# Optimization experiments

Hardware: AMD Instinct MI355X
Metric: run time of the kernel (lower is better)

## Reference

```python
import jax, jax.numpy as jnp
import numpy as np

N_NODES = 100000


def _gcn_conv(h, src, dst, W, b, n_nodes):
    """PyG GCNConv with add_self_loops=True, symmetric normalization.
    out = D^-1/2 (A + I) D^-1/2 (h W) + b, aggregating src->dst."""
    h = h @ W  # transform first (out_dim <= in_dim), as PyG does
    ones = jnp.ones(src.shape[0], dtype=h.dtype)
    deg = jax.ops.segment_sum(ones, dst, num_segments=n_nodes) + 1.0  # +1 self loop
    dinv = jax.lax.rsqrt(deg)
    coef = dinv[src] * dinv[dst]  # per-edge norm
    agg = jax.ops.segment_sum(h[src] * coef[:, None], dst, num_segments=n_nodes)
    agg = agg + h * (dinv * dinv)[:, None]  # self-loop term: dinv_i^2 * h_i
    return agg + b


def setup_inputs() -> dict:
    key = jax.random.key(0)
    k1, k2, k3, k4 = jax.random.split(key, 4)
    x = jax.random.normal(k1, (N_NODES, 256), dtype=jnp.float32)
    edge_index = jax.random.randint(k2, (2, 1600000), 0, N_NODES, dtype=jnp.int64)
    W1 = jax.random.normal(k3, (256, 128), dtype=jnp.float32) * (1.0 / np.sqrt(256))
    b1 = jnp.zeros((128,), dtype=jnp.float32)
    W2 = jax.random.normal(k4, (128, 64), dtype=jnp.float32) * (1.0 / np.sqrt(128))
    b2 = jnp.zeros((64,), dtype=jnp.float32)
    return {"x": x, "edge_index": edge_index, "W1": W1, "b1": b1, "W2": W2, "b2": b2}


def reference(x, edge_index, W1, b1, W2, b2):
    src, dst = edge_index[0], edge_index[1]
    h = jax.nn.relu(_gcn_conv(x, src, dst, W1, b1, N_NODES))
    # dropout is identity in eval mode
    h = _gcn_conv(h, src, dst, W2, b2, N_NODES)
    return jax.nn.log_softmax(h, axis=1)
```

## Files before the change

### kernel.cpp

```cpp
#include <hip/hip_runtime.h>
#include <hip/hip_bf16.h>


#define N_NODES 100000
#define F_IN 256
#define F_MID 128
#define F_OUT 64

#define BSHIFT 8
#define BNODES 256
#define NBUCKETS ((N_NODES + BNODES - 1) / BNODES)
#define BCAP 6144
#define EPB 4096

typedef __attribute__((ext_vector_type(8))) short short8;
typedef __attribute__((ext_vector_type(4))) float f32x4;

__device__ inline ushort bf16_rne(float f) {
    uint u = __float_as_uint(f);
    u += 0x7FFF + ((u >> 16) & 1);
    return (ushort)(u >> 16);
}
__device__ inline float lo16(uint r) { return __uint_as_float(r << 16); }
__device__ inline float hi16(uint r) { return __uint_as_float(r & 0xffff0000u); }
__device__ inline uint pack_bf2(float a, float b) {
    return (uint)bf16_rne(a) | ((uint)bf16_rne(b) << 16);
}

__global__ __launch_bounds__(256)
void bucket_sort_kernel(const uint* __restrict__ ebuf, const int* __restrict__ bcur,
                        int* __restrict__ ssrc, int* __restrict__ rs, int* __restrict__ cnt,
                        float* __restrict__ dinv, int n) {
    __shared__ uint eL[BCAP];
    __shared__ int  sLoc[BCAP];
    __shared__ int hist[BNODES], ps[BNODES];
    int b = blockIdx.x, t = threadIdx.x;
    int nb = bcur[b];
    if (nb > BCAP) nb = BCAP;
    for (int i = t; i < nb; i += 256) eL[i] = ebuf[(size_t)b * BCAP + i];
    hist[t] = 0;
    __syncthreads();
    for (int i = t; i < nb; i += 256) atomicAdd(&hist[eL[i] >> 17], 1);
    __syncthreads();
    ps[t] = hist[t];
    __syncthreads();
#pragma unroll
    for (int off = 1; off < BNODES; off <<= 1) {
        int v = (t >= off) ? ps[t - off] : 0;
        __syncthreads();
        ps[t] += v;
        __syncthreads();
    }
    int excl = ps[t] - hist[t];
    int node = b * BNODES + t;
    if (node < n) {
        rs[node] = b * BCAP + excl;
        cnt[node] = hist[t];
        dinv[node] = 1.0f / sqrtf((float)hist[t] + 1.0f);
    }
    __syncthreads();
    ps[t] = excl;
    __syncthreads();
    for (int i = t; i < nb; i += 256) {
        uint e = eL[i];
        int d = e >> 17;
        int p = atomicAdd(&ps[d], 1);
        sLoc[p] = (int)(e & 0x1FFFF);
    }
    __syncthreads();
    for (int i = t; i < nb; i += 256) ssrc[(size_t)b * BCAP + i] = sLoc[i];
}

__global__ __launch_bounds__(256)
void wprep_kernel(const float* __restrict__ W1, const float* __restrict__ W2,
                  short8* __restrict__ W1f, short8* __restrict__ W2f) {
    int b = blockIdx.x;
    if (b < 16) {
        int f = b * 256 + threadIdx.x;
        int k0 = f >> 9, nt = (f >> 6) & 7, ln = f & 63;
        int kbase = k0 * 32 + (ln >> 4) * 8;
        int n = nt * 16 + (ln & 15);
        short8 fr;
#pragma unroll
        for (int j = 0; j < 8; ++j) fr[j] = (short)bf16_rne(W1[(kbase + j) * F_MID + n]);
        W1f[f] = fr;
    } else {
        int f = (b - 16) * 256 + threadIdx.x;
        int k0 = f >> 8, nt = (f >> 6) & 3, ln = f & 63;
        int kbase = k0 * 32 + (ln >> 4) * 8;
        int n = nt * 16 + (ln & 15);
        short8 fr;
#pragma unroll
        for (int j = 0; j < 8; ++j) fr[j] = (short)bf16_rne(W2[(kbase + j) * F_OUT + n]);
        W2f[f] = fr;
    }
}

__global__ __launch_bounds__(512, 4)
void sg_kernel(const int* __restrict__ src, const int* __restrict__ dst,
               int* __restrict__ bcur, uint* __restrict__ ebuf, int E,
               const float* __restrict__ A, const short8* __restrict__ Wf,
               ushort* __restrict__ C, int M, int nScat) {
    __shared__ __align__(16) char smemRaw[32768];
    int t = threadIdx.x;

    if ((int)blockIdx.x < nScat) {
        int* hist = (int*)smemRaw;
        int* ps   = hist + 512;
        int* cur  = ps + 512;
        int* base = cur + 512;
        uint*   eLoc = (uint*)(base + NBUCKETS);
        ushort* bLoc = (ushort*)(eLoc + EPB);

        int e0 = blockIdx.x * EPB;
        int e1 = e0 + EPB; if (e1 > E) e1 = E;
        int ne = e1 - e0;

        hist[t] = 0;
        __syncthreads();
        for (int i = t; i < ne; i += 512) atomicAdd(&hist[dst[e0 + i] >> BSHIFT], 1);
        __syncthreads();
        ps[t] = hist[t];
        __syncthreads();
#pragma unroll
        for (int off = 1; off < 512; off <<= 1) {
            int v = (t >= off) ? ps[t - off] : 0;
            __syncthreads();
            ps[t] += v;
            __syncthreads();
        }
        int ex = ps[t] - hist[t];
        ps[t] = ex; cur[t] = ex;
        __syncthreads();
        for (int i = t; i < ne; i += 512) {
            int d = dst[e0 + i], s = src[e0 + i];
            int b = d >> BSHIFT;
            int p = atomicAdd(&cur[b], 1);
            eLoc[p] = ((uint)(d & (BNODES - 1)) << 17) | (uint)s;
            bLoc[p] = (ushort)b;
        }
        __syncthreads();
        for (int b = t; b < NBUCKETS; b += 512) {
            int h = hist[b];
            base[b] = h ? atomicAdd(&bcur[b], h) : 0;
        }
        __syncthreads();
        for (int i = t; i < ne; i += 512) {
            int b = bLoc[i];
            int d = base[b] + (i - ps[b]);
            if (d < BCAP) ebuf[(size_t)b * BCAP + d] = eLoc[i];
        }
        return;
    }

    ushort* Ab = (ushort*)smemRaw;
    int lane = t & 63, w = t >> 6;
    int bx = blockIdx.x - nScat;
    int m0 = bx * 128;

    int o0 = t * 2;
    int srow = o0 >> 3;
    int gr = m0 + srow; if (gr >= M) gr = m0;
    int cl0 = o0 & 7, cl1 = cl0 + 1;
    int cg0 = cl0 ^ (srow & 7), cg1 = cl1 ^ (srow & 7);
    const float* arow = &A[(size_t)gr * F_IN];

    float4 rv[2][2];
    rv[0][0] = ((const float4*)(arow + cg0 * 8))[0];
    rv[0][1] = ((const float4*)(arow + cg0 * 8))[1];
    rv[1][0] = ((const float4*)(arow + cg1 * 8))[0];
    rv[1][1] = ((const float4*)(arow + cg1 * 8))[1];

    {
        short8 pk;
        pk[0] = (short)bf16_rne(rv[0][0].x); pk[1] = (short)bf16_rne(rv[0][0].y);
        pk[2] = (short)bf16_rne(rv[0][0].z); pk[3] = (short)bf16_rne(rv[0][0].w);
        pk[4] = (short)bf16_rne(rv[0][1].x); pk[5] = (short)bf16_rne(rv[0][1].y);
        pk[6] = (short)bf16_rne(rv[0][1].z); pk[7] = (short)bf16_rne(rv[0][1].w);
        *(short8*)&Ab[o0 * 8] = pk;
        pk[0] = (short)bf16_rne(rv[1][0].x); pk[1] = (short)bf16_rne(rv[1][0].y);
        pk[2] = (short)bf16_rne(rv[1][0].z); pk[3] = (short)bf16_rne(rv[1][0].w);
        pk[4] = (short)bf16_rne(rv[1][1].x); pk[5] = (short)bf16_rne(rv[1][1].y);
        pk[6] = (short)bf16_rne(rv[1][1].z); pk[7] = (short)bf16_rne(rv[1][1].w);
        *(short8*)&Ab[(o0 + 1) * 8] = pk;
    }
    __syncthreads();

    f32x4 acc[8];
#pragma unroll
    for (int nt = 0; nt < 8; ++nt) acc[nt] = (f32x4){0.f, 0.f, 0.f, 0.f};

    int arow16 = w * 16 + (lane & 15);
    int asw = arow16 & 7;
    int abase = arow16 * 8;

#pragma unroll
    for (int kc = 0; kc < 4; ++kc) {
        int b = kc & 1;
        if (kc < 3) {
            const float* s0 = arow + (kc + 1) * 64 + cg0 * 8;
            const float* s1 = arow + (kc + 1) * 64 + cg1 * 8;
            rv[0][0] = ((const float4*)s0)[0];
            rv[0][1] = ((const float4*)s0)[1];
            rv[1][0] = ((const float4*)s1)[0];
            rv[1][1] = ((const float4*)s1)[1];
            asm volatile("" ::: "memory");
        }
#pragma unroll
        for (int kk = 0; kk < 2; ++kk) {
            int k0 = kc * 2 + kk;
            int c = kk * 4 + (lane >> 4);
            short8 af = *(const short8*)&Ab[b * 8192 + (abase + (c ^ asw)) * 8];
#pragma unroll
            for (int nt = 0; nt < 8; ++nt) {
                short8 bfr = Wf[(k0 * 8 + nt) * 64 + lane];
                acc[nt] = __builtin_amdgcn_mfma_f32_16x16x32_bf16(af, bfr, acc[nt], 0, 0, 0);
            }
        }
        if (kc < 3) {
            short8 pk;
            pk[0] = (short)bf16_rne(rv[0][0].x); pk[1] = (short)bf16_rne(rv[0][0].y);
            pk[2] = (short)bf16_rne(rv[0][0].z); pk[3] = (short)bf16_rne(rv[0][0].w);
            pk[4] = (short)bf16_rne(rv[0][1].x); pk[5] = (short)bf16_rne(rv[0][1].y);
            pk[6] = (short)bf16_rne(rv[0][1].z); pk[7] = (short)bf16_rne(rv[0][1].w);
            *(short8*)&Ab[(b ^ 1) * 8192 + o0 * 8] = pk;
            pk[0] = (short)bf16_rne(rv[1][0].x); pk[1] = (short)bf16_rne(rv[1][0].y);
            pk[2] = (short)bf16_rne(rv[1][0].z); pk[3] = (short)bf16_rne(rv[1][0].w);
            pk[4] = (short)bf16_rne(rv[1][1].x); pk[5] = (short)bf16_rne(rv[1][1].y);
            pk[6] = (short)bf16_rne(rv[1][1].z); pk[7] = (short)bf16_rne(rv[1][1].w);
            *(short8*)&Ab[(b ^ 1) * 8192 + (o0 + 1) * 8] = pk;
        }
        __syncthreads();
    }

#pragma unroll
    for (int i = 0; i < 4; ++i) {
        int r = m0 + w * 16 + (lane >> 4) * 4 + i;
        if (r < M) {
#pragma unroll
            for (int nt = 0; nt < 8; ++nt)
                C[(size_t)r * F_MID + nt * 16 + (lane & 15)] = bf16_rne(acc[nt][i]);
        }
    }
}

__global__ __launch_bounds__(256)
void agg1f_kernel(const uint4* __restrict__ h, const int* __restrict__ rs,
                  const int* __restrict__ cnt, const int* __restrict__ ssrc,
                  const float* __restrict__ dinv, const float* __restrict__ bias,
                  const short8* __restrict__ W2f, ushort* __restrict__ h2, int n) {
    __shared__ __align__(16) ushort rowsL[16][136];
    int w = threadIdx.x >> 6, lane = threadIdx.x & 63;
    int q = lane >> 4, c16 = lane & 15;
    int nbase = blockIdx.x * 16;
    const float4* b4 = (const float4*)bias;
    float4 b0 = b4[c16 * 2], b1v = b4[c16 * 2 + 1];

#pragma unroll
    for (int i = 0; i < 4; ++i) {
        int node = nbase + w * 4 + i;
        bool nOk = (node < n);
        int start = nOk ? rs[node] : 0;
        int c = nOk ? cnt[node] : 0;
        float dn = nOk ? dinv[node] : 0.f;
        float a[8];
#pragma unroll
        for (int k = 0; k < 8; ++k) a[k] = 0.f;

        for (int base = 0; base < c; base += 16) {
            bool p[4];
            int s[4];
            float ds[4];
            uint4 r[4];
#pragma unroll
            for (int j = 0; j < 4; ++j) {
                int e = base + j * 4 + q;
                p[j] = e < c;
                if (p[j]) s[j] = ssrc[start + e];
            }
#pragma unroll
            for (int j = 0; j < 4; ++j) {
                if (p[j]) {
                    r[j] = h[(size_t)s[j] * 16 + c16];
                    ds[j] = dinv[s[j]];
                }
            }
#pragma unroll
            for (int j = 0; j < 4; ++j) {
                if (p[j]) {
                    a[0] = fmaf(ds[j], lo16(r[j].x), a[0]); a[1] = fmaf(ds[j], hi16(r[j].x), a[1]);
                    a[2] = fmaf(ds[j], lo16(r[j].y), a[2]); a[3] = fmaf(ds[j], hi16(r[j].y), a[3]);
                    a[4] = fmaf(ds[j], lo16(r[j].z), a[4]); a[5] = fmaf(ds[j], hi16(r[j].z), a[5]);
                    a[6] = fmaf(ds[j], lo16(r[j].w), a[6]); a[7] = fmaf(ds[j], hi16(r[j].w), a[7]);
                }
            }
        }
#pragma unroll
        for (int k = 0; k < 8; ++k) {
            a[k] += __shfl_xor(a[k], 16);
            a[k] += __shfl_xor(a[k], 32);
        }
        if (q == 0) {
            short8 pk;
            if (nOk) {
                uint4 sr = h[(size_t)node * 16 + c16];
                float o0 = fmaxf(fmaf(dn, fmaf(dn, lo16(sr.x), a[0]), b0.x), 0.f);
                float o1 = fmaxf(fmaf(dn, fmaf(dn, hi16(sr.x), a[1]), b0.y), 0.f);
                float o2 = fmaxf(fmaf(dn, fmaf(dn, lo16(sr.y), a[2]), b0.z), 0.f);
                float o3 = fmaxf(fmaf(dn, fmaf(dn, hi16(sr.y), a[3]), b0.w), 0.f);
                float o4 = fmaxf(fmaf(dn, fmaf(dn, lo16(sr.z), a[4]), b1v.x), 0.f);
                float o5 = fmaxf(fmaf(dn, fmaf(dn, hi16(sr.z), a[5]), b1v.y), 0.f);
                float o6 = fmaxf(fmaf(dn, fmaf(dn, lo16(sr.w), a[6]), b1v.z), 0.f);
                float o7 = fmaxf(fmaf(dn, fmaf(dn, hi16(sr.w), a[7]), b1v.w), 0.f);
                pk[0] = (short)bf16_rne(o0); pk[1] = (short)bf16_rne(o1);
                pk[2] = (short)bf16_rne(o2); pk[3] = (short)bf16_rne(o3);
                pk[4] = (short)bf16_rne(o4); pk[5] = (short)bf16_rne(o5);
                pk[6] = (short)bf16_rne(o6); pk[7] = (short)bf16_rne(o7);
            } else {
                pk = (short8){0, 0, 0, 0, 0, 0, 0, 0};
            }
            *(short8*)&rowsL[w * 4 + i][c16 * 8] = pk;
        }
    }
    __syncthreads();

    f32x4 acc = (f32x4){0.f, 0.f, 0.f, 0.f};
    int ar = lane & 15;
#pragma unroll
    for (int k0 = 0; k0 < 4; ++k0) {
        short8 af = *(const short8*)&rowsL[ar][k0 * 32 + (lane >> 4) * 8];
        short8 bfr = W2f[(k0 * 4 + w) * 64 + lane];
        acc = __builtin_amdgcn_mfma_f32_16x16x32_bf16(af, bfr, acc, 0, 0, 0);
    }
#pragma unroll
    for (int i = 0; i < 4; ++i) {
        int r = (lane >> 4) * 4 + i;
        int node = nbase + r;
        if (node < n) {
            float dv = dinv[node];
            h2[(size_t)node * F_OUT + w * 16 + (lane & 15)] = bf16_rne(dv * acc[i]);
        }
    }
}

__global__ __launch_bounds__(256)
void agg2_kernel(const uint2* __restrict__ h, const int* __restrict__ rs,
                 const int* __restrict__ cnt, const int* __restrict__ ssrc,
                 const float* __restrict__ dinv, const float* __restrict__ bias,
                 float4* __restrict__ out4, int n) {
    int w = threadIdx.x >> 6, lane = threadIdx.x & 63;
    int q = lane >> 4, c16 = lane & 15;
    int nodeA = blockIdx.x * 8 + w * 2;
    int nodeB = nodeA + 1;
    bool okA = (nodeA < n), okB = (nodeB < n);
    if (!okA) return;
    int startA = rs[nodeA], cA = cnt[nodeA];
    int startB = okB ? rs[nodeB] : 0, cB = okB ? cnt[nodeB] : 0;
    float dnA = dinv[nodeA];
    float dnB = okB ? dinv[nodeB] : 0.f;
    float aA[4], aB[4];
#pragma unroll
    for (int i = 0; i < 4; ++i) { aA[i] = 0.f; aB[i] = 0.f; }

    int cm = cA > cB ? cA : cB;
    for (int base = 0; base < cm; base += 16) {
        bool pA[4], pB[4];
        int sA[4], sB[4];
        uint2 rA[4], rB[4];
#pragma unroll
        for (int j = 0; j < 4; ++j) {
            int e = base + j * 4 + q;
            pA[j] = e < cA;
            pB[j] = e < cB;
            if (pA[j]) sA[j] = ssrc[startA + e];
            if (pB[j]) sB[j] = ssrc[startB + e];
        }
#pragma unroll
        for (int j = 0; j < 4; ++j) {
            if (pA[j]) rA[j] = h[(size_t)sA[j] * 16 + c16];
            if (pB[j]) rB[j] = h[(size_t)sB[j] * 16 + c16];
        }
#pragma unroll
        for (int j = 0; j < 4; ++j) {
            if (pA[j]) {
                aA[0] += lo16(rA[j].x); aA[1] += hi16(rA[j].x);
                aA[2] += lo16(rA[j].y); aA[3] += hi16(rA[j].y);
            }
            if (pB[j]) {
                aB[0] += lo16(rB[j].x); aB[1] += hi16(rB[j].x);
                aB[2] += lo16(rB[j].y); aB[3] += hi16(rB[j].y);
            }
        }
    }
#pragma unroll
    for (int i = 0; i < 4; ++i) {
        aA[i] += __shfl_xor(aA[i], 16);
        aA[i] += __shfl_xor(aA[i], 32);
        aB[i] += __shfl_xor(aB[i], 16);
        aB[i] += __shfl_xor(aB[i], 32);
    }
    float4 bv = ((const float4*)bias)[c16];
    {
        uint2 sr = h[(size_t)nodeA * 16 + c16];
        float v0 = fmaf(dnA, aA[0] + lo16(sr.x), bv.x);
        float v1 = fmaf(dnA, aA[1] + hi16(sr.x), bv.y);
        float v2 = fmaf(dnA, aA[2] + lo16(sr.y), bv.z);
        float v3 = fmaf(dnA, aA[3] + hi16(sr.y), bv.w);
        float m = fmaxf(fmaxf(v0, v1), fmaxf(v2, v3));
#pragma unroll
        for (int off = 1; off < 16; off <<= 1) m = fmaxf(m, __shfl_xor(m, off));
        float ssum = expf(v0 - m) + expf(v1 - m) + expf(v2 - m) + expf(v3 - m);
#pragma unroll
        for (int off = 1; off < 16; off <<= 1) ssum += __shfl_xor(ssum, off);
        float lg = m + logf(ssum);
        if (q == 0) out4[(size_t)nodeA * 16 + c16] = make_float4(v0 - lg, v1 - lg, v2 - lg, v3 - lg);
    }
    if (okB) {
        uint2 sr = h[(size_t)nodeB * 16 + c16];
        float v0 = fmaf(dnB, aB[0] + lo16(sr.x), bv.x);
        float v1 = fmaf(dnB, aB[1] + hi16(sr.x), bv.y);
        float v2 = fmaf(dnB, aB[2] + lo16(sr.y), bv.z);
        float v3 = fmaf(dnB, aB[3] + hi16(sr.y), bv.w);
        float m = fmaxf(fmaxf(v0, v1), fmaxf(v2, v3));
#pragma unroll
        for (int off = 1; off < 16; off <<= 1) m = fmaxf(m, __shfl_xor(m, off));
        float ssum = expf(v0 - m) + expf(v1 - m) + expf(v2 - m) + expf(v3 - m);
#pragma unroll
        for (int off = 1; off < 16; off <<= 1) ssum += __shfl_xor(ssum, off);
        float lg = m + logf(ssum);
        if (q == 0) out4[(size_t)nodeB * 16 + c16] = make_float4(v0 - lg, v1 - lg, v2 - lg, v3 - lg);
    }
}


extern "C" void kernel_launch(void* const* d_in, const int* in_sizes, int n_in,
                              void* d_out, int out_size, void* d_ws, size_t ws_size,
                              hipStream_t stream) {
    const float* x  = (const float*)d_in[0];
    const int*   ei = (const int*)d_in[1];
    const float* W1 = (const float*)d_in[2];
    const float* b1 = (const float*)d_in[3];
    const float* W2 = (const float*)d_in[4];
    const float* b2 = (const float*)d_in[5];
    float* out = (float*)d_out;

    const int N = N_NODES;
    const int E = in_sizes[1] / 2;
    const int* src = ei;
    const int* dst = ei + E;

    char* ws = (char*)d_ws;
    size_t off = 0;
    auto alloc = [&](size_t bytes) {
        char* p = ws + off;
        off = (off + bytes + 255) & ~(size_t)255;
        return p;
    };
    int*    bcur   = (int*)alloc(NBUCKETS * 4);
    int*    rs     = (int*)alloc(N * 4);
    int*    cnt    = (int*)alloc(N * 4);
    float*  dinv   = (float*)alloc(N * 4);
    short8* W1f    = (short8*)alloc(4096 * 16);
    short8* W2f    = (short8*)alloc(1024 * 16);
    uint*   ebuf   = (uint*)alloc((size_t)NBUCKETS * BCAP * 4);
    int*    ssrc   = (int*)alloc((size_t)NBUCKETS * BCAP * 4);
    uint*   h1     = (uint*)alloc((size_t)N * 64 * 4);
    ushort* h2     = (ushort*)alloc((size_t)N * 64 * 2);

    const int nScat       = (E + EPB - 1) / EPB;
    const int nAgg1Blocks = (N + 15) / 16;
    const int nAgg2Blocks = (N + 7) / 8;
    const int nTiles      = (N + 127) / 128;

    hipMemsetAsync(bcur, 0, NBUCKETS * 4, stream);
    wprep_kernel<<<20, 256, 0, stream>>>(W1, W2, W1f, W2f);

    sg_kernel<<<nScat + nTiles, 512, 0, stream>>>(src, dst, bcur, ebuf, E,
                                                  x, W1f, (ushort*)h1, N, nScat);
    bucket_sort_kernel<<<NBUCKETS, 256, 0, stream>>>(ebuf, bcur, ssrc, rs, cnt, dinv, N);

    agg1f_kernel<<<nAgg1Blocks, 256, 0, stream>>>((const uint4*)h1, rs, cnt, ssrc, dinv, b1,
                                                  W2f, h2, N);
    agg2_kernel<<<nAgg2Blocks, 256, 0, stream>>>((const uint2*)h2, rs, cnt, ssrc, dinv, b2,
                                                 (float4*)out, N);
}
```

Baseline: 336.2 us.

## Split GEMM1 tiles across scatter and bucket-sort kernels to overlap work

The layer-1 GEMM tiles were previously all co-launched with the edge-scatter blocks. Now 480 tiles stay in the scatter kernel and the rest run inside the bucket-sort launch, which is widened to 512 threads with a larger shared buffer. The aim is to balance both launches so neither leaves the GPU idle on its irregular phase. The risk is that the 51KB shared allocation in the second kernel lowers occupancy for its GEMM blocks, and the 480 split point is hard-coded.

```diff
diff --git a/kernel.cpp b/kernel.cpp
--- a/kernel.cpp
+++ b/kernel.cpp
@@ -23,139 +23,12 @@
 }
 __device__ inline float lo16(uint r) { return __uint_as_float(r << 16); }
 __device__ inline float hi16(uint r) { return __uint_as_float(r & 0xffff0000u); }
-__device__ inline uint pack_bf2(float a, float b) {
-    return (uint)bf16_rne(a) | ((uint)bf16_rne(b) << 16);
-}
-
-__global__ __launch_bounds__(256)
-void bucket_sort_kernel(const uint* __restrict__ ebuf, const int* __restrict__ bcur,
-                        int* __restrict__ ssrc, int* __restrict__ rs, int* __restrict__ cnt,
-                        float* __restrict__ dinv, int n) {
-    __shared__ uint eL[BCAP];
-    __shared__ int  sLoc[BCAP];
-    __shared__ int hist[BNODES], ps[BNODES];
-    int b = blockIdx.x, t = threadIdx.x;
-    int nb = bcur[b];
-    if (nb > BCAP) nb = BCAP;
-    for (int i = t; i < nb; i += 256) eL[i] = ebuf[(size_t)b * BCAP + i];
-    hist[t] = 0;
-    __syncthreads();
-    for (int i = t; i < nb; i += 256) atomicAdd(&hist[eL[i] >> 17], 1);
-    __syncthreads();
-    ps[t] = hist[t];
-    __syncthreads();
-#pragma unroll
-    for (int off = 1; off < BNODES; off <<= 1) {
-        int v = (t >= off) ? ps[t - off] : 0;
-        __syncthreads();
-        ps[t] += v;
-        __syncthreads();
-    }
-    int excl = ps[t] - hist[t];
-    int node = b * BNODES + t;
-    if (node < n) {
-        rs[node] = b * BCAP + excl;
-        cnt[node] = hist[t];
-        dinv[node] = 1.0f / sqrtf((float)hist[t] + 1.0f);
-    }
-    __syncthreads();
-    ps[t] = excl;
-    __syncthreads();
-    for (int i = t; i < nb; i += 256) {
-        uint e = eL[i];
-        int d = e >> 17;
-        int p = atomicAdd(&ps[d], 1);
-        sLoc[p] = (int)(e & 0x1FFFF);
-    }
-    __syncthreads();
-    for (int i = t; i < nb; i += 256) ssrc[(size_t)b * BCAP + i] = sLoc[i];
-}
-
-__global__ __launch_bounds__(256)
-void wprep_kernel(const float* __restrict__ W1, const float* __restrict__ W2,
-                  short8* __restrict__ W1f, short8* __restrict__ W2f) {
-    int b = blockIdx.x;
-    if (b < 16) {
-        int f = b * 256 + threadIdx.x;
-        int k0 = f >> 9, nt = (f >> 6) & 7, ln = f & 63;
-        int kbase = k0 * 32 + (ln >> 4) * 8;
-        int n = nt * 16 + (ln & 15);
-        short8 fr;
-#pragma unroll
-        for (int j = 0; j < 8; ++j) fr[j] = (short)bf16_rne(W1[(kbase + j) * F_MID + n]);
-        W1f[f] = fr;
-    } else {
-        int f = (b - 16) * 256 + threadIdx.x;
-        int k0 = f >> 8, nt = (f >> 6) & 3, ln = f & 63;
-        int kbase = k0 * 32 + (ln >> 4) * 8;
-        int n = nt * 16 + (ln & 15);
-        short8 fr;
-#pragma unroll
-        for (int j = 0; j < 8; ++j) fr[j] = (short)bf16_rne(W2[(kbase + j) * F_OUT + n]);
-        W2f[f] = fr;
-    }
-}
-
-__global__ __launch_bounds__(512, 4)
-void sg_kernel(const int* __restrict__ src, const int* __restrict__ dst,
-               int* __restrict__ bcur, uint* __restrict__ ebuf, int E,
-               const float* __restrict__ A, const short8* __restrict__ Wf,
-               ushort* __restrict__ C, int M, int nScat) {
-    __shared__ __align__(16) char smemRaw[32768];
-    int t = threadIdx.x;
-
-    if ((int)blockIdx.x < nScat) {
-        int* hist = (int*)smemRaw;
-        int* ps   = hist + 512;
-        int* cur  = ps + 512;
-        int* base = cur + 512;
-        uint*   eLoc = (uint*)(base + NBUCKETS);
-        ushort* bLoc = (ushort*)(eLoc + EPB);
-
-        int e0 = blockIdx.x * EPB;
-        int e1 = e0 + EPB; if (e1 > E) e1 = E;
-        int ne = e1 - e0;
-
-        hist[t] = 0;
-        __syncthreads();
-        for (int i = t; i < ne; i += 512) atomicAdd(&hist[dst[e0 + i] >> BSHIFT], 1);
-        __syncthreads();
-        ps[t] = hist[t];
-        __syncthreads();
-#pragma unroll
-        for (int off = 1; off < 512; off <<= 1) {
-            int v = (t >= off) ? ps[t - off] : 0;
-            __syncthreads();
-            ps[t] += v;
-            __syncthreads();
-        }
-        int ex = ps[t] - hist[t];
-        ps[t] = ex; cur[t] = ex;
-        __syncthreads();
-        for (int i = t; i < ne; i += 512) {
-            int d = dst[e0 + i], s = src[e0 + i];
-            int b = d >> BSHIFT;
-            int p = atomicAdd(&cur[b], 1);
-            eLoc[p] = ((uint)(d & (BNODES - 1)) << 17) | (uint)s;
-            bLoc[p] = (ushort)b;
-        }
-        __syncthreads();
-        for (int b = t; b < NBUCKETS; b += 512) {
-            int h = hist[b];
-            base[b] = h ? atomicAdd(&bcur[b], h) : 0;
-        }
-        __syncthreads();
-        for (int i = t; i < ne; i += 512) {
-            int b = bLoc[i];
-            int d = base[b] + (i - ps[b]);
-            if (d < BCAP) ebuf[(size_t)b * BCAP + d] = eLoc[i];
-        }
-        return;
-    }
-
+
+__device__ __forceinline__ void gemm1_role(int bx, int t, const float* __restrict__ A,
+                                           const short8* __restrict__ Wf,
+                                           ushort* __restrict__ C, int M, char* smemRaw) {
     ushort* Ab = (ushort*)smemRaw;
     int lane = t & 63, w = t >> 6;
-    int bx = blockIdx.x - nScat;
     int m0 = bx * 128;
 
     int o0 = t * 2;
@@ -241,6 +114,144 @@
             for (int nt = 0; nt < 8; ++nt)
                 C[(size_t)r * F_MID + nt * 16 + (lane & 15)] = bf16_rne(acc[nt][i]);
         }
+    }
+}
+
+__global__ __launch_bounds__(512, 4)
+void sg1_kernel(const int* __restrict__ src, const int* __restrict__ dst,
+                int* __restrict__ bcur, uint* __restrict__ ebuf, int E,
+                const float* __restrict__ A, const short8* __restrict__ Wf,
+                ushort* __restrict__ C, int M, int nScat) {
+    __shared__ __align__(16) char smemRaw[32768];
+    int t = threadIdx.x;
+
+    if ((int)blockIdx.x < nScat) {
+        int* hist = (int*)smemRaw;
+        int* ps   = hist + 512;
+        int* cur  = ps + 512;
+        int* base = cur + 512;
+        uint*   eLoc = (uint*)(base + NBUCKETS);
+        ushort* bLoc = (ushort*)(eLoc + EPB);
+
+        int e0 = blockIdx.x * EPB;
+        int e1 = e0 + EPB; if (e1 > E) e1 = E;
+        int ne = e1 - e0;
+
+        hist[t] = 0;
+        __syncthreads();
+        for (int i = t; i < ne; i += 512) atomicAdd(&hist[dst[e0 + i] >> BSHIFT], 1);
+        __syncthreads();
+        ps[t] = hist[t];
+        __syncthreads();
+#pragma unroll
+        for (int off = 1; off < 512; off <<= 1) {
+            int v = (t >= off) ? ps[t - off] : 0;
+            __syncthreads();
+            ps[t] += v;
+            __syncthreads();
+        }
+        int ex = ps[t] - hist[t];
+        ps[t] = ex; cur[t] = ex;
+        __syncthreads();
+        for (int i = t; i < ne; i += 512) {
+            int d = dst[e0 + i], s = src[e0 + i];
+            int b = d >> BSHIFT;
+            int p = atomicAdd(&cur[b], 1);
+            eLoc[p] = ((uint)(d & (BNODES - 1)) << 17) | (uint)s;
+            bLoc[p] = (ushort)b;
+        }
+        __syncthreads();
+        for (int b = t; b < NBUCKETS; b += 512) {
+            int h = hist[b];
+            base[b] = h ? atomicAdd(&bcur[b], h) : 0;
+        }
+        __syncthreads();
+        for (int i = t; i < ne; i += 512) {
+            int b = bLoc[i];
+            int d = base[b] + (i - ps[b]);
+            if (d < BCAP) ebuf[(size_t)b * BCAP + d] = eLoc[i];
+        }
+        return;
+    }
+    gemm1_role((int)blockIdx.x - nScat, t, A, Wf, C, M, smemRaw);
+}
+
+__global__ __launch_bounds__(512, 4)
+void sg2_kernel(const uint* __restrict__ ebuf, const int* __restrict__ bcur,
+                int* __restrict__ ssrc, int* __restrict__ rs, int* __restrict__ cnt,
+                float* __restrict__ dinv, int n,
+                const float* __restrict__ A, const short8* __restrict__ Wf,
+                ushort* __restrict__ C, int M, int nSort, int tileBase) {
+    __shared__ __align__(16) char smemRaw[51200];
+    int t = threadIdx.x;
+
+    if ((int)blockIdx.x < nSort) {
+        uint* eL   = (uint*)smemRaw;
+        int*  sLoc = (int*)(eL + BCAP);
+        int*  hist = sLoc + BCAP;
+        int*  ps   = hist + BNODES;
+        int b = blockIdx.x;
+        int nb = bcur[b];
+        if (nb > BCAP) nb = BCAP;
+        for (int i = t; i < nb; i += 512) eL[i] = ebuf[(size_t)b * BCAP + i];
+        if (t < BNODES) hist[t] = 0;
+        __syncthreads();
+        for (int i = t; i < nb; i += 512) atomicAdd(&hist[eL[i] >> 17], 1);
+        __syncthreads();
+        if (t < BNODES) ps[t] = hist[t];
+        __syncthreads();
+#pragma unroll
+        for (int off = 1; off < BNODES; off <<= 1) {
+            int v = (t >= off && t < BNODES) ? ps[t - off] : 0;
+            __syncthreads();
+            if (t < BNODES) ps[t] += v;
+            __syncthreads();
+        }
+        if (t < BNODES) {
+            int excl = ps[t] - hist[t];
+            int node = b * BNODES + t;
+            if (node < n) {
+                rs[node] = b * BCAP + excl;
+                cnt[node] = hist[t];
+                dinv[node] = 1.0f / sqrtf((float)hist[t] + 1.0f);
+            }
+            ps[t] = excl;
+        }
+        __syncthreads();
+        for (int i = t; i < nb; i += 512) {
+            uint e = eL[i];
+            int p = atomicAdd(&ps[e >> 17], 1);
+            sLoc[p] = (int)(e & 0x1FFFF);
+        }
+        __syncthreads();
+        for (int i = t; i < nb; i += 512) ssrc[(size_t)b * BCAP + i] = sLoc[i];
+        return;
+    }
+    gemm1_role(tileBase + (int)blockIdx.x - nSort, t, A, Wf, C, M, smemRaw);
+}
+
+__global__ __launch_bounds__(256)
+void wprep_kernel(const float* __restrict__ W1, const float* __restrict__ W2,
+                  short8* __restrict__ W1f, short8* __restrict__ W2f) {
+    int b = blockIdx.x;
+    if (b < 16) {
+        int f = b * 256 + threadIdx.x;
+        int k0 = f >> 9, nt = (f >> 6) & 7, ln = f & 63;
+        int kbase = k0 * 32 + (ln >> 4) * 8;
+        int n = nt * 16 + (ln & 15);
+        short8 fr;
+#pragma unroll
+        for (int j = 0; j < 8; ++j) fr[j] = (short)bf16_rne(W1[(kbase + j) * F_MID + n]);
+        W1f[f] = fr;
+    } else {
+        int f = (b - 16) * 256 + threadIdx.x;
+        int k0 = f >> 8, nt = (f >> 6) & 3, ln = f & 63;
+        int kbase = k0 * 32 + (ln >> 4) * 8;
+        int n = nt * 16 + (ln & 15);
+        short8 fr;
+#pragma unroll
+        for (int j = 0; j < 8; ++j) fr[j] = (short)bf16_rne(W2[(kbase + j) * F_OUT + n]);
+        W2f[f] = fr;
     }
 }
 
@@ -471,13 +482,16 @@
     const int nAgg1Blocks = (N + 15) / 16;
     const int nAgg2Blocks = (N + 7) / 8;
     const int nTiles      = (N + 127) / 128;
+    const int T1          = 480;
+    const int T2          = nTiles - T1;
 
     hipMemsetAsync(bcur, 0, NBUCKETS * 4, stream);
     wprep_kernel<<<20, 256, 0, stream>>>(W1, W2, W1f, W2f);
 
-    sg_kernel<<<nScat + nTiles, 512, 0, stream>>>(src, dst, bcur, ebuf, E,
-                                                  x, W1f, (ushort*)h1, N, nScat);
-    bucket_sort_kernel<<<NBUCKETS, 256, 0, stream>>>(ebuf, bcur, ssrc, rs, cnt, dinv, N);
+    sg1_kernel<<<nScat + T1, 512, 0, stream>>>(src, dst, bcur, ebuf, E,
+                                               x, W1f, (ushort*)h1, N, nScat);
+    sg2_kernel<<<NBUCKETS + T2, 512, 0, stream>>>(ebuf, bcur, ssrc, rs, cnt, dinv, N,
+                                                  x, W1f, (ushort*)h1, N, NBUCKETS, T1);
 
     agg1f_kernel<<<nAgg1Blocks, 256, 0, stream>>>((const uint4*)h1, rs, cnt, ssrc, dinv, b1,
                                                   W2f, h2, N);
```

Measured after the change: 338.7 us. Within noise of the previous version (+0.8%).
